# Kernel optimization log

Measured on AMD Instinct MI355X. Metric: run time of the kernel, lower is better.

Reference implementation:

```python
import jax, jax.numpy as jnp
import numpy as np


def setup_inputs() -> dict:
    key = jax.random.key(0)
    ks = jax.random.split(key, 9)
    B, T, C, H = 4, 2048, 1024, 16
    hd = C // H  # 64
    s = 0.02
    return {
        "x": jax.random.normal(ks[0], (B, T, C), dtype=jnp.float32),
        "Wq": jax.random.normal(ks[1], (H, C, hd), dtype=jnp.float32) * s,
        "bq": jax.random.normal(ks[2], (H, hd), dtype=jnp.float32) * s,
        "Wk": jax.random.normal(ks[3], (H, C, hd), dtype=jnp.float32) * s,
        "bk": jax.random.normal(ks[4], (H, hd), dtype=jnp.float32) * s,
        "Wv": jax.random.normal(ks[5], (H, C, hd), dtype=jnp.float32) * s,
        "bv": jax.random.normal(ks[6], (H, hd), dtype=jnp.float32) * s,
        "Wp": jax.random.normal(ks[7], (C, C), dtype=jnp.float32) * s,
        "bp": jax.random.normal(ks[8], (C,), dtype=jnp.float32) * s,
    }


def reference(x, Wq, bq, Wk, bk, Wv, bv, Wp, bp):
    B, T, C = x.shape
    # per-head projections, batched over heads: [B,H,T,hd]
    q = jnp.einsum('btc,hcd->bhtd', x, Wq) + bq[None, :, None, :]
    k = jnp.einsum('btc,hcd->bhtd', x, Wk) + bk[None, :, None, :]
    v = jnp.einsum('btc,hcd->bhtd', x, Wv) + bv[None, :, None, :]
    # NOTE: original scales by full embed dim C (not head_size) -- faithful quirk
    scale = jnp.asarray(C, x.dtype) ** -0.5
    wei = jnp.einsum('bhtd,bhsd->bhts', q, k) * scale  # [B,H,T,T]
    causal = jnp.tril(jnp.ones((T, T), dtype=bool))
    wei = jnp.where(causal, wei, jnp.asarray(-jnp.inf, wei.dtype))
    wei = jax.nn.softmax(wei, axis=-1)
    out = jnp.einsum('bhts,bhsd->bhtd', wei, v)  # [B,H,T,hd]
    # concat heads along feature dim -> [B,T,C]
    out = out.transpose(0, 2, 1, 3).reshape(B, T, C)
    return out @ Wp + bp
```

## Files before the change

kernel.cpp:

```cpp
#include <hip/hip_runtime.h>
#include <hip/hip_bf16.h>
#include <stdint.h>


typedef unsigned short u16;
typedef __attribute__((ext_vector_type(4))) float f32x4;
typedef __attribute__((ext_vector_type(8))) __bf16 bf16x8;
typedef __attribute__((ext_vector_type(2))) __bf16 bf16x2;

#define DEV static __device__ __forceinline__

DEV u16 f2bf(float f) {
  uint32_t u = __builtin_bit_cast(uint32_t, f);
  return (u16)((u + 0x7FFFu + ((u >> 16) & 1u)) >> 16);
}

DEV uint pack2(float a, float b) {
  bf16x2 v;
  v.x = (__bf16)a;
  v.y = (__bf16)b;
  return __builtin_bit_cast(uint, v);
}

#if __has_builtin(__builtin_amdgcn_exp2f)
DEV float fexp2(float x) { return __builtin_amdgcn_exp2f(x); }
#else
DEV float fexp2(float x) { return __expf(x * 0.69314718056f); }
#endif

DEV void gload_lds16(const void* g, void* lds) {
  auto gp = reinterpret_cast<const __attribute__((address_space(1))) uint32_t*>(
      reinterpret_cast<uintptr_t>(g));
  auto lp = reinterpret_cast<__attribute__((address_space(3))) uint32_t*>(
      static_cast<uint32_t>(reinterpret_cast<uintptr_t>(lds)));
  __builtin_amdgcn_global_load_lds(gp, lp, 16, 0, 0);
}

DEV f32x4 mfma16(bf16x8 a, bf16x8 b, f32x4 c) {
  return __builtin_amdgcn_mfma_f32_16x16x32_bf16(a, b, c, 0, 0, 0);
}

#define LD8(p) (*reinterpret_cast<const bf16x8*>(p))
#define LDU4(p) (*reinterpret_cast<const uint4*>(p))


__global__ void cvt_x_kernel(const float* __restrict__ x, u16* __restrict__ xb, int n8) {
  int i = blockIdx.x * blockDim.x + threadIdx.x;
  int stride = gridDim.x * blockDim.x;
  for (; i < n8; i += stride) {
    const float4* xp = reinterpret_cast<const float4*>(x) + 2 * (size_t)i;
    float4 a = xp[0], b = xp[1];
    uint4 o;
    o.x = pack2(a.x, a.y);
    o.y = pack2(a.z, a.w);
    o.z = pack2(b.x, b.y);
    o.w = pack2(b.z, b.w);
    reinterpret_cast<uint4*>(xb)[i] = o;
  }
}

__global__ void cvt_wqkv_kernel(const float* __restrict__ Wq, const float* __restrict__ Wk,
                                const float* __restrict__ Wv, const float* __restrict__ bq,
                                const float* __restrict__ bk, const float* __restrict__ bv,
                                u16* __restrict__ wt, float* __restrict__ biasq) {
  __shared__ u16 tle[64 * 72];
  const int tid = threadIdx.x;
  const int ct = blockIdx.x;
  const int h = blockIdx.y;
  const int which = blockIdx.z;
  const float* W = (which == 0) ? Wq : (which == 1) ? Wk : Wv;
  const float* Bb = (which == 0) ? bq : (which == 1) ? bk : bv;
  const float scl = (which == 0) ? 0.045084220027780106f : 1.0f;
#pragma unroll
  for (int i = 0; i < 4; ++i) {
    int idx = i * 256 + tid;
    int c_l = idx >> 4, d4 = (idx & 15) * 4;
    float4 v = *reinterpret_cast<const float4*>(&W[((size_t)(h * 1024 + ct * 64 + c_l)) * 64 + d4]);
    tle[(d4 + 0) * 72 + c_l] = f2bf(v.x * scl);
    tle[(d4 + 1) * 72 + c_l] = f2bf(v.y * scl);
    tle[(d4 + 2) * 72 + c_l] = f2bf(v.z * scl);
    tle[(d4 + 3) * 72 + c_l] = f2bf(v.w * scl);
  }
  __syncthreads();
#pragma unroll
  for (int i = 0; i < 2; ++i) {
    int idx = i * 256 + tid;
    int d_o = idx >> 3, c8 = (idx & 7) * 8;
    uint4 v = LDU4(&tle[d_o * 72 + c8]);
    *reinterpret_cast<uint4*>(&wt[(size_t)(which * 1024 + h * 64 + d_o) * 1024 + ct * 64 + c8]) = v;
  }
  if (ct == 0 && tid < 64) biasq[which * 1024 + h * 64 + tid] = Bb[h * 64 + tid] * scl;
}

__global__ void cvt_wp_kernel(const float* __restrict__ Wp, u16* __restrict__ wpt) {
  __shared__ u16 tle[64 * 72];
  const int tid = threadIdx.x;
  const int ct = blockIdx.x;
  const int nt = blockIdx.y;
#pragma unroll
  for (int i = 0; i < 4; ++i) {
    int idx = i * 256 + tid;
    int c_l = idx >> 4, n4 = (idx & 15) * 4;
    float4 v = *reinterpret_cast<const float4*>(&Wp[(size_t)(ct * 64 + c_l) * 1024 + nt * 64 + n4]);
    tle[(n4 + 0) * 72 + c_l] = f2bf(v.x);
    tle[(n4 + 1) * 72 + c_l] = f2bf(v.y);
    tle[(n4 + 2) * 72 + c_l] = f2bf(v.z);
    tle[(n4 + 3) * 72 + c_l] = f2bf(v.w);
  }
  __syncthreads();
#pragma unroll
  for (int i = 0; i < 2; ++i) {
    int idx = i * 256 + tid;
    int n_o = idx >> 3, c8 = (idx & 7) * 8;
    uint4 v = LDU4(&tle[n_o * 72 + c8]);
    *reinterpret_cast<uint4*>(&wpt[(size_t)(nt * 64 + n_o) * 1024 + ct * 64 + c8]) = v;
  }
}

__global__ __launch_bounds__(256)
void transpose_v_kernel(const u16* __restrict__ qkv, u16* __restrict__ vT) {
  __shared__ alignas(16) u16 tle[64 * 72];
  const int tid = threadIdx.x;
  const int tt = blockIdx.x;
  const int h = blockIdx.y;
  const int bb = blockIdx.z;
  const size_t rbase = ((size_t)bb * 2048 + tt * 64) * 3072 + 2048 + h * 64;
#pragma unroll
  for (int i = 0; i < 2; ++i) {
    int idx = i * 256 + tid;
    int s = idx >> 3, c8 = (idx & 7) * 8;
    *reinterpret_cast<uint4*>(&tle[s * 72 + c8]) = LDU4(&qkv[rbase + (size_t)s * 3072 + c8]);
  }
  __syncthreads();
#pragma unroll
  for (int i = 0; i < 2; ++i) {
    int idx = i * 256 + tid;
    int d = idx >> 3, cb = idx & 7;
    uint4 o;
    o.x = (uint)tle[(2 * cb + 0) * 72 + d] | ((uint)tle[(16 + 2 * cb + 0) * 72 + d] << 16);
    o.y = (uint)tle[(32 + 2 * cb + 0) * 72 + d] | ((uint)tle[(48 + 2 * cb + 0) * 72 + d] << 16);
    o.z = (uint)tle[(2 * cb + 1) * 72 + d] | ((uint)tle[(16 + 2 * cb + 1) * 72 + d] << 16);
    o.w = (uint)tle[(32 + 2 * cb + 1) * 72 + d] | ((uint)tle[(48 + 2 * cb + 1) * 72 + d] << 16);
    *reinterpret_cast<uint4*>(
        &vT[((size_t)(bb * 16 + h) * 64 + d) * 2048 + tt * 64 + cb * 8]) = o;
  }
}


template <bool OUT_F32>
__global__ __launch_bounds__(256)
void gemm_kernel(const u16* __restrict__ A, const u16* __restrict__ Bt,
                 const float* __restrict__ bias, void* __restrict__ Cout,
                 int M, int N, int K) {
  __shared__ alignas(16) u16 As[128 * 32];
  __shared__ alignas(16) u16 Bs[128 * 32];
  const int tid = threadIdx.x;
  const int lane = tid & 63;
  const int wave = tid >> 6;
  const int wr = wave >> 1, wc = wave & 1;
  const int m0 = blockIdx.x * 128;
  const int n0 = blockIdx.y * 128;

  const int srow = tid >> 2;
  const int scol = (tid & 3) * 8;
  const u16* gA0 = A + (size_t)(m0 + srow) * K + scol;
  const u16* gA1 = gA0 + (size_t)64 * K;
  const u16* gB0 = Bt + (size_t)(n0 + srow) * K + scol;
  const u16* gB1 = gB0 + (size_t)64 * K;
  char* ldsA = (char*)As + tid * 16;
  char* ldsB = (char*)Bs + tid * 16;

  f32x4 acc[4][4] = {};
  const int fr = lane & 15;
  const int kg = (lane >> 4) * 8;

  for (int k0 = 0; k0 < K; k0 += 32) {
    gload_lds16(gA0 + k0, ldsA);
    gload_lds16(gA1 + k0, ldsA + 4096);
    gload_lds16(gB0 + k0, ldsB);
    gload_lds16(gB1 + k0, ldsB + 4096);
    asm volatile("s_waitcnt vmcnt(0)" ::: "memory");
    __syncthreads();
    bf16x8 af[4], bfr[4];
#pragma unroll
    for (int f = 0; f < 4; ++f)
      af[f] = LD8(&As[(wr * 64 + f * 16 + fr) * 32 + kg]);
#pragma unroll
    for (int f = 0; f < 4; ++f)
      bfr[f] = LD8(&Bs[(wc * 64 + f * 16 + fr) * 32 + kg]);
#pragma unroll
    for (int i = 0; i < 4; ++i)
#pragma unroll
      for (int j = 0; j < 4; ++j)
        acc[i][j] = mfma16(af[i], bfr[j], acc[i][j]);
    __syncthreads();
  }

#pragma unroll
  for (int i = 0; i < 4; ++i) {
    const int rbase = m0 + wr * 64 + i * 16 + ((lane >> 4) * 4);
#pragma unroll
    for (int j = 0; j < 4; ++j) {
      const int col = n0 + wc * 64 + j * 16 + fr;
      const float bv = bias[col];
#pragma unroll
      for (int r = 0; r < 4; ++r) {
        float v = acc[i][j][r] + bv;
        size_t off = (size_t)(rbase + r) * N + col;
        if constexpr (OUT_F32) reinterpret_cast<float*>(Cout)[off] = v;
        else                   reinterpret_cast<u16*>(Cout)[off] = f2bf(v);
      }
    }
  }
}


__global__ __launch_bounds__(256, 4)
void attn_kernel(const u16* __restrict__ qkv, const u16* __restrict__ vT,
                 u16* __restrict__ obuf) {
  __shared__ alignas(16) u16 Ks[64 * 72];
  __shared__ alignas(16) u16 Vs[64 * 72];
  __shared__ alignas(16) u16 Ps[4][16 * 72];

  const int tid = threadIdx.x;
  const int lane = tid & 63;
  const int wave = tid >> 6;

  const int gid = blockIdx.x;
  const int xcd = gid & 7;
  const int jj = gid >> 3;
  const int g = xcd * 8 + (jj >> 4);
  const int pair = jj & 15;
  const int bb = g >> 4;
  const int h = g & 15;

  const size_t baseQ = (size_t)bb * 2048 * 3072 + h * 64;
  const size_t baseK = baseQ + 1024;
  const size_t baseVt = (size_t)(bb * 16 + h) * 64 * 2048;

  const int fr = lane & 15;
  const int kg8 = (lane >> 4) * 8;
  const int qw16 = wave * 16;
  const int r4 = (lane >> 4) * 4;

  const int rr = tid >> 3;
  const int cc8 = (tid & 7) * 8;
  const size_t gK0 = (size_t)rr * 3072 + cc8;
  const size_t gK1 = (size_t)(rr + 32) * 3072 + cc8;
  const size_t gV0 = (size_t)rr * 2048 + cc8;
  const size_t gV1 = (size_t)(rr + 32) * 2048 + cc8;
  const int l0 = rr * 72 + cc8;
  const int l1 = (rr + 32) * 72 + cc8;
  u16* __restrict__ Pw = &Ps[wave][0];

  for (int half = 0; half < 2; ++half) {
    const int qt = half ? (31 - pair) : pair;
    const int q0 = qt * 64;
    const int nt = qt + 1;

    const u16* qrow = &qkv[baseQ + (size_t)(q0 + qw16 + fr) * 3072 + kg8];
    bf16x8 aq0 = LD8(qrow);
    bf16x8 aq1 = LD8(qrow + 32);

    float lsum0 = 0.f, lsum1 = 0.f, lsum2 = 0.f, lsum3 = 0.f;
    f32x4 o0 = {}, o1 = {}, o2 = {}, o3 = {};

    uint4 kr0 = LDU4(&qkv[baseK + gK0]);
    uint4 kr1 = LDU4(&qkv[baseK + gK1]);
    uint4 vr0 = LDU4(&vT[baseVt + gV0]);
    uint4 vr1 = LDU4(&vT[baseVt + gV1]);

    for (int t = 0; t < nt; ++t) {
      __syncthreads();
      *reinterpret_cast<uint4*>(&Ks[l0]) = kr0;
      *reinterpret_cast<uint4*>(&Ks[l1]) = kr1;
      *reinterpret_cast<uint4*>(&Vs[l0]) = vr0;
      *reinterpret_cast<uint4*>(&Vs[l1]) = vr1;
      if (t + 1 < nt) {
        const u16* nk = &qkv[baseK + (size_t)(t + 1) * 64 * 3072];
        const u16* nv = &vT[baseVt + (size_t)(t + 1) * 64];
        kr0 = LDU4(nk + gK0);
        kr1 = LDU4(nk + gK1);
        vr0 = LDU4(nv + gV0);
        vr1 = LDU4(nv + gV1);
      }
      __syncthreads();

      f32x4 s0 = {}, s1 = {}, s2 = {}, s3 = {};
      {
        bf16x8 b;
        __builtin_amdgcn_s_setprio(1);
        b = LD8(&Ks[(fr) * 72 + kg8]);           s0 = mfma16(aq0, b, s0);
        b = LD8(&Ks[(16 + fr) * 72 + kg8]);      s1 = mfma16(aq0, b, s1);
        b = LD8(&Ks[(32 + fr) * 72 + kg8]);      s2 = mfma16(aq0, b, s2);
        b = LD8(&Ks[(48 + fr) * 72 + kg8]);      s3 = mfma16(aq0, b, s3);
        b = LD8(&Ks[(fr) * 72 + 32 + kg8]);      s0 = mfma16(aq1, b, s0);
        b = LD8(&Ks[(16 + fr) * 72 + 32 + kg8]); s1 = mfma16(aq1, b, s1);
        b = LD8(&Ks[(32 + fr) * 72 + 32 + kg8]); s2 = mfma16(aq1, b, s2);
        b = LD8(&Ks[(48 + fr) * 72 + 32 + kg8]); s3 = mfma16(aq1, b, s3);
        __builtin_amdgcn_s_setprio(0);
      }

      const bool diag = (t == nt - 1);
#define SM_ROW(r)                                                              \
      {                                                                        \
        const int qg = qw16 + r4 + r;                                          \
        float p0 = fexp2(s0[r]);                                               \
        float p1 = fexp2(s1[r]);                                               \
        float p2 = fexp2(s2[r]);                                               \
        float p3 = fexp2(s3[r]);                                               \
        if (diag) {                                                            \
          if (fr > qg) p0 = 0.f;                                               \
          if (fr + 16 > qg) p1 = 0.f;                                          \
          if (fr + 32 > qg) p2 = 0.f;                                          \
          if (fr + 48 > qg) p3 = 0.f;                                          \
        }                                                                      \
        lsum##r += (p0 + p1) + (p2 + p3);                                      \
        uint2 w;                                                               \
        w.x = pack2(p0, p1);                                                   \
        w.y = pack2(p2, p3);                                                   \
        *reinterpret_cast<uint2*>(&Pw[(r4 + r) * 72 + fr * 4]) = w;            \
      }
      SM_ROW(0) SM_ROW(1) SM_ROW(2) SM_ROW(3)
#undef SM_ROW

      {
        bf16x8 pf0 = LD8(&Pw[fr * 72 + kg8]);
        bf16x8 v;
        __builtin_amdgcn_s_setprio(1);
        v = LD8(&Vs[(fr) * 72 + kg8]);           o0 = mfma16(pf0, v, o0);
        v = LD8(&Vs[(16 + fr) * 72 + kg8]);      o1 = mfma16(pf0, v, o1);
        v = LD8(&Vs[(32 + fr) * 72 + kg8]);      o2 = mfma16(pf0, v, o2);
        v = LD8(&Vs[(48 + fr) * 72 + kg8]);      o3 = mfma16(pf0, v, o3);
        bf16x8 pf1 = LD8(&Pw[fr * 72 + 32 + kg8]);
        v = LD8(&Vs[(fr) * 72 + 32 + kg8]);      o0 = mfma16(pf1, v, o0);
        v = LD8(&Vs[(16 + fr) * 72 + 32 + kg8]); o1 = mfma16(pf1, v, o1);
        v = LD8(&Vs[(32 + fr) * 72 + 32 + kg8]); o2 = mfma16(pf1, v, o2);
        v = LD8(&Vs[(48 + fr) * 72 + 32 + kg8]); o3 = mfma16(pf1, v, o3);
        __builtin_amdgcn_s_setprio(0);
      }
    }

#define EPI(r)                                                                 \
    {                                                                          \
      float s = lsum##r;                                                       \
      s += __shfl_xor(s, 1);                                                   \
      s += __shfl_xor(s, 2);                                                   \
      s += __shfl_xor(s, 4);                                                   \
      s += __shfl_xor(s, 8);                                                   \
      const float inv = 1.0f / s;                                              \
      const int qg = q0 + qw16 + r4 + r;                                       \
      const size_t rowoff = ((size_t)bb * 2048 + qg) * 1024 + h * 64;          \
      obuf[rowoff + fr] = f2bf(o0[r] * inv);                                   \
      obuf[rowoff + 16 + fr] = f2bf(o1[r] * inv);                              \
      obuf[rowoff + 32 + fr] = f2bf(o2[r] * inv);                              \
      obuf[rowoff + 48 + fr] = f2bf(o3[r] * inv);                              \
    }
    EPI(0) EPI(1) EPI(2) EPI(3)
#undef EPI
  }
}


extern "C" void kernel_launch(void* const* d_in, const int* in_sizes, int n_in,
                              void* d_out, int out_size, void* d_ws, size_t ws_size,
                              hipStream_t stream) {
  const float* x  = (const float*)d_in[0];
  const float* Wq = (const float*)d_in[1];
  const float* bq = (const float*)d_in[2];
  const float* Wk = (const float*)d_in[3];
  const float* bk = (const float*)d_in[4];
  const float* Wv = (const float*)d_in[5];
  const float* bv = (const float*)d_in[6];
  const float* Wp = (const float*)d_in[7];
  const float* bp = (const float*)d_in[8];

  char* ws = (char*)d_ws;
  size_t off = 0;
  auto alloc = [&](size_t bytes) -> void* {
    void* p = ws + off;
    off += (bytes + 255) & ~(size_t)255;
    return p;
  };
  u16*   xb     = (u16*)  alloc((size_t)8192 * 1024 * 2);
  u16*   wqkv_t = (u16*)  alloc((size_t)3072 * 1024 * 2);
  float* biasq  = (float*)alloc((size_t)3072 * 4);
  u16*   wpt    = (u16*)  alloc((size_t)1024 * 1024 * 2);
  u16*   qkv    = (u16*)  alloc((size_t)8192 * 3072 * 2);
  u16*   obuf   = (u16*)  alloc((size_t)8192 * 1024 * 2);
  u16*   vT     = xb;
  (void)ws_size; (void)in_sizes; (void)n_in; (void)out_size;

  cvt_x_kernel<<<2048, 256, 0, stream>>>(x, xb, 8192 * 1024 / 8);
  cvt_wqkv_kernel<<<dim3(16, 16, 3), 256, 0, stream>>>(Wq, Wk, Wv, bq, bk, bv, wqkv_t, biasq);
  cvt_wp_kernel<<<dim3(16, 16), 256, 0, stream>>>(Wp, wpt);
  gemm_kernel<false><<<dim3(64, 24), 256, 0, stream>>>(xb, wqkv_t, biasq, qkv, 8192, 3072, 1024);
  transpose_v_kernel<<<dim3(32, 16, 4), 256, 0, stream>>>(qkv, vT);
  attn_kernel<<<1024, 256, 0, stream>>>(qkv, vT, obuf);
  gemm_kernel<true><<<dim3(64, 8), 256, 0, stream>>>(obuf, wpt, bp, d_out, 8192, 1024, 1024);
}
```

Before: 183.5 us.

## Replace GEMM with double-buffered 128x256 8-wave pipelined kernel

Replaces the simple single-buffered 128x128 GEMM with a 512-thread kernel that uses 128x256 tiles and a K-step of 64. A and B tiles are double-buffered in LDS and loaded directly from global memory into LDS. Global loads for upcoming K-steps are interleaved with the MFMA phases and gated by explicit vmcnt/lgkmcnt waits, barriers and s_setprio. A swizzled block-index mapping is added to improve L2 reuse. The aim is to hide memory latency and raise MFMA utilization in both projection GEMMs. In exchange, the kernel needs about 96KB of LDS per block, which limits occupancy, and it depends on fragile hand-placed wait counts.

Measured after the change: 196.7 us. 7.2% more time.

```diff
diff --git a/kernel.cpp b/kernel.cpp
--- a/kernel.cpp
+++ b/kernel.cpp
@@ -38,6 +38,12 @@
 
 DEV f32x4 mfma16(bf16x8 a, bf16x8 b, f32x4 c) {
   return __builtin_amdgcn_mfma_f32_16x16x32_bf16(a, b, c, 0, 0, 0);
+}
+
+DEV void bar() {
+  asm volatile("" ::: "memory");
+  __builtin_amdgcn_s_barrier();
+  asm volatile("" ::: "memory");
 }
 
 #define LD8(p) (*reinterpret_cast<const bf16x8*>(p))
@@ -148,65 +154,138 @@
 
 
 template <bool OUT_F32>
-__global__ __launch_bounds__(256)
-void gemm_kernel(const u16* __restrict__ A, const u16* __restrict__ Bt,
-                 const float* __restrict__ bias, void* __restrict__ Cout,
-                 int M, int N, int K) {
-  __shared__ alignas(16) u16 As[128 * 32];
-  __shared__ alignas(16) u16 Bs[128 * 32];
+__global__ __launch_bounds__(512, 2)
+void gemm8p_kernel(const u16* __restrict__ A, const u16* __restrict__ Bt,
+                   const float* __restrict__ bias, void* __restrict__ Cout,
+                   int M, int N, int K, int nbn) {
+  __shared__ alignas(16) u16 LAs[2][128 * 64];
+  __shared__ alignas(16) u16 LBs[2][256 * 64];
+
   const int tid = threadIdx.x;
   const int lane = tid & 63;
   const int wave = tid >> 6;
-  const int wr = wave >> 1, wc = wave & 1;
-  const int m0 = blockIdx.x * 128;
-  const int n0 = blockIdx.y * 128;
-
-  const int srow = tid >> 2;
-  const int scol = (tid & 3) * 8;
-  const u16* gA0 = A + (size_t)(m0 + srow) * K + scol;
-  const u16* gA1 = gA0 + (size_t)64 * K;
-  const u16* gB0 = Bt + (size_t)(n0 + srow) * K + scol;
-  const u16* gB1 = gB0 + (size_t)64 * K;
-  char* ldsA = (char*)As + tid * 16;
-  char* ldsB = (char*)Bs + tid * 16;
+  const int wm = wave >> 2;
+  const int wn = wave & 3;
+  const int fr = lane & 15;
+  const int kg8 = (lane >> 4) * 8;
+  const int r4 = (lane >> 4) * 4;
+
+  const int nwg = gridDim.x;
+  const int swz = (blockIdx.x & 7) * (nwg >> 3) + (blockIdx.x >> 3);
+  const int m0 = (swz / nbn) * 128;
+  const int n0 = (swz % nbn) * 256;
+
+  const int NT = K >> 6;
+
+  const int srow = tid >> 3;
+  const int scol = (tid & 7) * 8;
+  const size_t aOff = (size_t)(m0 + srow) * K + scol;
+  const size_t bOff = (size_t)(n0 + srow) * K + scol;
+  const int ldst = tid * 8;
+
+  auto stageA = [&](int kt, int q, u16* la) {
+    gload_lds16(A + aOff + (size_t)q * 64 * K + (size_t)kt * 64, la + q * 4096 + ldst);
+  };
+  auto stageB = [&](int kt, int q, u16* lb) {
+    gload_lds16(Bt + bOff + (size_t)q * 64 * K + (size_t)kt * 64, lb + q * 4096 + ldst);
+  };
 
   f32x4 acc[4][4] = {};
-  const int fr = lane & 15;
-  const int kg = (lane >> 4) * 8;
-
-  for (int k0 = 0; k0 < K; k0 += 32) {
-    gload_lds16(gA0 + k0, ldsA);
-    gload_lds16(gA1 + k0, ldsA + 4096);
-    gload_lds16(gB0 + k0, ldsB);
-    gload_lds16(gB1 + k0, ldsB + 4096);
-    asm volatile("s_waitcnt vmcnt(0)" ::: "memory");
-    __syncthreads();
-    bf16x8 af[4], bfr[4];
-#pragma unroll
-    for (int f = 0; f < 4; ++f)
-      af[f] = LD8(&As[(wr * 64 + f * 16 + fr) * 32 + kg]);
-#pragma unroll
-    for (int f = 0; f < 4; ++f)
-      bfr[f] = LD8(&Bs[(wc * 64 + f * 16 + fr) * 32 + kg]);
-#pragma unroll
-    for (int i = 0; i < 4; ++i)
-#pragma unroll
-      for (int j = 0; j < 4; ++j)
-        acc[i][j] = mfma16(af[i], bfr[j], acc[i][j]);
-    __syncthreads();
-  }
-
-#pragma unroll
-  for (int i = 0; i < 4; ++i) {
-    const int rbase = m0 + wr * 64 + i * 16 + ((lane >> 4) * 4);
-#pragma unroll
-    for (int j = 0; j < 4; ++j) {
-      const int col = n0 + wc * 64 + j * 16 + fr;
+
+  {
+    u16* la = LAs[0];
+    u16* lb = LBs[0];
+    stageA(0, 0, la); stageA(0, 1, la);
+    stageB(0, 0, lb); stageB(0, 1, lb); stageB(0, 2, lb); stageB(0, 3, lb);
+    if (NT > 1) {
+      u16* lb1 = LBs[1];
+      stageB(1, 0, lb1); stageB(1, 1, lb1); stageB(1, 2, lb1); stageB(1, 3, lb1);
+      asm volatile("s_waitcnt vmcnt(4)" ::: "memory");
+    } else {
+      asm volatile("s_waitcnt vmcnt(0)" ::: "memory");
+    }
+  }
+  bar();
+
+  for (int kt = 0; kt < NT; ++kt) {
+    u16* la = LAs[kt & 1];
+    u16* lb = LBs[kt & 1];
+    u16* la_n = LAs[(kt & 1) ^ 1];
+    const bool st1 = (kt + 1 < NT);
+    const bool st2 = (kt + 2 < NT);
+
+    bf16x8 bs0[4], bs1[4];
+
+    bf16x8 a0k0 = LD8(&la[(wm * 64 + 0 + fr) * 64 + 0 + kg8]);
+    bf16x8 a0k1 = LD8(&la[(wm * 64 + 0 + fr) * 64 + 32 + kg8]);
+    bf16x8 a1k0 = LD8(&la[(wm * 64 + 16 + fr) * 64 + 0 + kg8]);
+    bf16x8 a1k1 = LD8(&la[(wm * 64 + 16 + fr) * 64 + 32 + kg8]);
+#pragma unroll
+    for (int n = 0; n < 4; ++n) bs0[n] = LD8(&lb[(wn * 64 + n * 16 + fr) * 64 + kg8]);
+    if (st1) { stageA(kt + 1, 0, la_n); stageA(kt + 1, 1, la_n); }
+    bar();
+    __builtin_amdgcn_s_setprio(1);
+#pragma unroll
+    for (int n = 0; n < 4; ++n) acc[0][n] = mfma16(a0k0, bs0[n], acc[0][n]);
+#pragma unroll
+    for (int n = 0; n < 4; ++n) acc[1][n] = mfma16(a1k0, bs0[n], acc[1][n]);
+    __builtin_amdgcn_s_setprio(0);
+    asm volatile("s_waitcnt lgkmcnt(0)" ::: "memory");
+    bar();
+
+#pragma unroll
+    for (int n = 0; n < 4; ++n) bs1[n] = LD8(&lb[(wn * 64 + n * 16 + fr) * 64 + 32 + kg8]);
+    bar();
+    __builtin_amdgcn_s_setprio(1);
+#pragma unroll
+    for (int n = 0; n < 4; ++n) acc[0][n] = mfma16(a0k1, bs1[n], acc[0][n]);
+#pragma unroll
+    for (int n = 0; n < 4; ++n) acc[1][n] = mfma16(a1k1, bs1[n], acc[1][n]);
+    __builtin_amdgcn_s_setprio(0);
+    asm volatile("s_waitcnt lgkmcnt(0)" ::: "memory");
+    bar();
+
+    bf16x8 a2k0 = LD8(&la[(wm * 64 + 32 + fr) * 64 + 0 + kg8]);
+    bf16x8 a2k1 = LD8(&la[(wm * 64 + 32 + fr) * 64 + 32 + kg8]);
+    bf16x8 a3k0 = LD8(&la[(wm * 64 + 48 + fr) * 64 + 0 + kg8]);
+    bf16x8 a3k1 = LD8(&la[(wm * 64 + 48 + fr) * 64 + 32 + kg8]);
+    if (st2) { stageB(kt + 2, 0, lb); stageB(kt + 2, 1, lb); }
+    bar();
+    __builtin_amdgcn_s_setprio(1);
+#pragma unroll
+    for (int n = 0; n < 4; ++n) acc[2][n] = mfma16(a2k0, bs0[n], acc[2][n]);
+#pragma unroll
+    for (int n = 0; n < 4; ++n) acc[3][n] = mfma16(a3k0, bs0[n], acc[3][n]);
+    __builtin_amdgcn_s_setprio(0);
+    asm volatile("s_waitcnt lgkmcnt(0)" ::: "memory");
+    bar();
+
+    if (st2) { stageB(kt + 2, 2, lb); stageB(kt + 2, 3, lb); }
+    if (st1) {
+      if (st2) asm volatile("s_waitcnt vmcnt(4)" ::: "memory");
+      else     asm volatile("s_waitcnt vmcnt(0)" ::: "memory");
+    }
+    bar();
+    __builtin_amdgcn_s_setprio(1);
+#pragma unroll
+    for (int n = 0; n < 4; ++n) acc[2][n] = mfma16(a2k1, bs1[n], acc[2][n]);
+#pragma unroll
+    for (int n = 0; n < 4; ++n) acc[3][n] = mfma16(a3k1, bs1[n], acc[3][n]);
+    __builtin_amdgcn_s_setprio(0);
+    bar();
+  }
+
+#pragma unroll
+  for (int m = 0; m < 4; ++m) {
+    const int row = m0 + wm * 64 + m * 16 + r4;
+#pragma unroll
+    for (int n = 0; n < 4; ++n) {
+      const int col = n0 + wn * 64 + n * 16 + fr;
       const float bv = bias[col];
 #pragma unroll
       for (int r = 0; r < 4; ++r) {
-        float v = acc[i][j][r] + bv;
-        size_t off = (size_t)(rbase + r) * N + col;
+        float v = acc[m][n][r] + bv;
+        size_t off = (size_t)(row + r) * N + col;
         if constexpr (OUT_F32) reinterpret_cast<float*>(Cout)[off] = v;
         else                   reinterpret_cast<u16*>(Cout)[off] = f2bf(v);
       }
@@ -394,8 +473,8 @@
   cvt_x_kernel<<<2048, 256, 0, stream>>>(x, xb, 8192 * 1024 / 8);
   cvt_wqkv_kernel<<<dim3(16, 16, 3), 256, 0, stream>>>(Wq, Wk, Wv, bq, bk, bv, wqkv_t, biasq);
   cvt_wp_kernel<<<dim3(16, 16), 256, 0, stream>>>(Wp, wpt);
-  gemm_kernel<false><<<dim3(64, 24), 256, 0, stream>>>(xb, wqkv_t, biasq, qkv, 8192, 3072, 1024);
+  gemm8p_kernel<false><<<768, 512, 0, stream>>>(xb, wqkv_t, biasq, qkv, 8192, 3072, 1024, 12);
   transpose_v_kernel<<<dim3(32, 16, 4), 256, 0, stream>>>(qkv, vT);
   attn_kernel<<<1024, 256, 0, stream>>>(qkv, vT, obuf);
-  gemm_kernel<true><<<dim3(64, 8), 256, 0, stream>>>(obuf, wpt, bp, d_out, 8192, 1024, 1024);
-}
+  gemm8p_kernel<true><<<256, 512, 0, stream>>>(obuf, wpt, bp, d_out, 8192, 1024, 1024, 4);
+}
```
